# Performance work log

Hardware: AMD Instinct MI355X
Metric: run time of the kernel (lower is better)

## Reference

```python
import jax, jax.numpy as jnp
import numpy as np

V0 = 32000  # medicine vocab; SOS = V0, END = V0 + 1
E = 1024    # emb_dim


def setup_inputs() -> dict:
    key = jax.random.key(0)
    ks = jax.random.split(key, 12)
    s = 0.02
    return {
        "input_diagnosis": jax.random.randint(ks[0], (128,), 0, 35501),
        "input_procedure": jax.random.randint(ks[1], (64,), 0, 35501),
        "input_medicine": jax.random.randint(ks[2], (128,), 0, 35501),
        "dec_tokens": jax.random.randint(ks[3], (64,), 0, V0),
        "enc_emb": jax.random.normal(ks[4], (35501, E), jnp.float32) * s,
        "dec_emb": jax.random.normal(ks[5], (V0 + 2, E), jnp.float32) * s,
        "attn_w": jax.random.normal(ks[6], (1, 2 * E), jnp.float32) * s,
        "attn_b": jnp.zeros((1,), jnp.float32),
        "gru_w_ih": jax.random.normal(ks[7], (3 * E, 2 * E), jnp.float32) * s,
        "gru_w_hh": jax.random.normal(ks[8], (3 * E, E), jnp.float32) * s,
        "gru_b_ih": jnp.zeros((3 * E,), jnp.float32),
        "gru_b_hh": jnp.zeros((3 * E,), jnp.float32),
        "out_w": jax.random.normal(ks[9], (V0 + 2, E), jnp.float32) * s,
        "out_b": jnp.zeros((V0 + 2,), jnp.float32),
    }


def reference(input_diagnosis, input_procedure, input_medicine, dec_tokens,
              enc_emb, dec_emb, attn_w, attn_b,
              gru_w_ih, gru_w_hh, gru_b_ih, gru_b_hh, out_w, out_b):
    # Context: concat of the three code-set embeddings -> [L, E]
    ctx = jnp.concatenate([enc_emb[input_diagnosis],
                           enc_emb[input_procedure],
                           enc_emb[input_medicine]], axis=0)
    # Teacher-forced decoder token sequence: [SOS] + targets -> [T]
    tokens = jnp.concatenate([jnp.array([V0], dec_tokens.dtype), dec_tokens])
    dec_x = dec_emb[tokens]  # [T, E]
    h0 = dec_x[0]            # hidden init = SOS embedding (hidden_state None branch)
    # Additive attention Linear(2E,1): split weight into hidden part / context part
    w_h = attn_w[0, :E]
    w_e = attn_w[0, E:]
    ctx_score = ctx @ w_e + attn_b[0]  # [L], precomputed once

    def step(h, x):
        scores = ctx_score + jnp.dot(h, w_h)          # [L]
        a = jax.nn.softmax(scores)
        c = a @ ctx                                    # [E] weighted context
        u = jnp.concatenate([c, x])                    # [2E] GRU input
        gi = gru_w_ih @ u + gru_b_ih
        gh = gru_w_hh @ h + gru_b_hh
        ir, iz, in_ = jnp.split(gi, 3)
        hr, hz, hn = jnp.split(gh, 3)
        r = jax.nn.sigmoid(ir + hr)
        z = jax.nn.sigmoid(iz + hz)
        n = jnp.tanh(in_ + r * hn)
        h_new = (1.0 - z) * n + z * h                  # PyTorch GRU cell
        logits = out_w @ jax.nn.relu(h_new) + out_b    # [V0+2]
        return h_new, logits

    _, logits = jax.lax.scan(step, h0, dec_x)          # [T, V0+2]
    return logits
```

## Files before the change

### kernel.cpp

```cpp
#include <hip/hip_runtime.h>
#include <hip/hip_cooperative_groups.h>

typedef unsigned long long u64;
#define V0TOK 32000
#define EDIM  1024

__device__ __forceinline__ float dot4(float4 a, float4 b) {
    return fmaf(a.x, b.x, fmaf(a.y, b.y, fmaf(a.z, b.z, a.w * b.w)));
}

__global__ __launch_bounds__(512, 1) void k_rnn(
    const int* __restrict__ diag, const int* __restrict__ proc,
    const int* __restrict__ med,  const int* __restrict__ dtok,
    const float* __restrict__ enc, const float* __restrict__ dec,
    const float* __restrict__ attw,
    const float* __restrict__ wih, const float* __restrict__ whh,
    const float* __restrict__ bih, const float* __restrict__ bhh,
    float* __restrict__ ctx_ws, float* __restrict__ c_ws,
    u64* __restrict__ hbuf, float* __restrict__ hrelu)
{
    const int b = blockIdx.x, tid = threadIdx.x;
    const int w = tid >> 6, l = tid & 63;

    __shared__ float Wx[24 * 1024];
    __shared__ float sm[320];
    __shared__ float red1[8], red2[8];
    __shared__ float hlds[1024];

    if (b < 4)
        __hip_atomic_store(&hbuf[b * 512 + tid], 0ull,
                           __ATOMIC_RELAXED, __HIP_MEMORY_SCOPE_AGENT);
    if (b < 40) {
        int i = 8*b + w;
        int ridx = (i < 128) ? diag[i] : (i < 192 ? proc[i-128] : med[i-192]);
        const float4* row = (const float4*)(enc + (size_t)ridx * EDIM);
        const float4* we  = (const float4*)(attw + EDIM);
        float p = 0.f;
        #pragma unroll
        for (int m = 0; m < 4; m++) p += dot4(row[l + 64*m], we[l + 64*m]);
        #pragma unroll
        for (int off = 32; off; off >>= 1) p += __shfl_xor(p, off);
        if (l == 0) ctx_ws[i] = p;
    }
    __threadfence();
    cooperative_groups::this_grid().sync();
    __threadfence();

    {
        float s1 = (tid < 320) ? ctx_ws[tid] : -1e30f;
        float mx = s1;
        #pragma unroll
        for (int off = 32; off; off >>= 1) mx = fmaxf(mx, __shfl_xor(mx, off));
        if (l == 0) red1[w] = mx;
        __syncthreads();
        mx = red1[0];
        #pragma unroll
        for (int k = 1; k < 8; k++) mx = fmaxf(mx, red1[k]);
        float e1 = (tid < 320) ? expf(s1 - mx) : 0.f;
        float ss = e1;
        #pragma unroll
        for (int off = 32; off; off >>= 1) ss += __shfl_xor(ss, off);
        if (l == 0) red2[w] = ss;
        __syncthreads();
        float tot = red2[0];
        #pragma unroll
        for (int k = 1; k < 8; k++) tot += red2[k];
        if (tid < 320) sm[tid] = e1 / tot;
        __syncthreads();

        int e = 8*b + w;
        float p = 0.f;
        for (int i = l; i < 320; i += 64) {
            int ridx = (i < 128) ? diag[i] : (i < 192 ? proc[i-128] : med[i-192]);
            p += sm[i] * enc[(size_t)ridx * EDIM + e];
        }
        #pragma unroll
        for (int off = 32; off; off >>= 1) p += __shfl_xor(p, off);
        if (l == 0) c_ws[e] = p;
    }
    __threadfence();
    cooperative_groups::this_grid().sync();
    __threadfence();

    const int jr = 8*b + w, jz = 1024 + jr, jn = 2048 + jr;

    {
        const float4* s_r = (const float4*)(wih + (size_t)jr * 2048 + 1024);
        const float4* s_z = (const float4*)(wih + (size_t)jz * 2048 + 1024);
        const float4* s_n = (const float4*)(wih + (size_t)jn * 2048 + 1024);
        float4* d_r = (float4*)(Wx + (0*8 + w) * 1024);
        float4* d_z = (float4*)(Wx + (1*8 + w) * 1024);
        float4* d_n = (float4*)(Wx + (2*8 + w) * 1024);
        #pragma unroll
        for (int m = 0; m < 4; m++) {
            d_r[l + 64*m] = s_r[l + 64*m];
            d_z[l + 64*m] = s_z[l + 64*m];
            d_n[l + 64*m] = s_n[l + 64*m];
        }
    }

    float4 whr[4], whz[4], whn[4];
    {
        const float4* qr = (const float4*)(whh + (size_t)jr * 1024);
        const float4* qz = (const float4*)(whh + (size_t)jz * 1024);
        const float4* qn = (const float4*)(whh + (size_t)jn * 1024);
        #pragma unroll
        for (int m = 0; m < 4; m++) { whr[m] = qr[l + 64*m]; whz[m] = qz[l + 64*m]; whn[m] = qn[l + 64*m]; }
    }

    float4 c4[4], h4[4];
    {
        const float4* cp = (const float4*)c_ws;
        const float4* hp = (const float4*)(dec + (size_t)V0TOK * EDIM);
        #pragma unroll
        for (int m = 0; m < 4; m++) { c4[m] = cp[l + 64*m]; h4[m] = hp[l + 64*m]; }
    }
    const float b_r  = bih[jr] + bhh[jr];
    const float b_z  = bih[jz] + bhh[jz];
    const float b_ni = bih[jn];
    const float b_nh = bhh[jn];

    float gic_r = 0.f, gic_z = 0.f, gic_n = 0.f;
    {
        const float4* pr = (const float4*)(wih + (size_t)jr * 2048);
        const float4* pz = (const float4*)(wih + (size_t)jz * 2048);
        const float4* pn = (const float4*)(wih + (size_t)jn * 2048);
        #pragma unroll
        for (int m = 0; m < 4; m++) {
            gic_r += dot4(pr[l + 64*m], c4[m]);
            gic_z += dot4(pz[l + 64*m], c4[m]);
            gic_n += dot4(pn[l + 64*m], c4[m]);
        }
    }

    __syncthreads();

    const float4* WxR = (const float4*)(Wx + (0*8 + w) * 1024);
    const float4* WxZ = (const float4*)(Wx + (1*8 + w) * 1024);
    const float4* WxN = (const float4*)(Wx + (2*8 + w) * 1024);

    int tokreg = dtok[l];

    float gxr = gic_r, gxz = gic_z, gxn = gic_n;
    #pragma unroll
    for (int m = 0; m < 4; m++) {
        gxr += dot4(WxR[l + 64*m], h4[m]);
        gxz += dot4(WxZ[l + 64*m], h4[m]);
        gxn += dot4(WxN[l + 64*m], h4[m]);
    }
    float4 xv[4];
    {
        int tok1 = __shfl(tokreg, 0);
        const float4* xp = (const float4*)(dec + (size_t)tok1 * EDIM);
        #pragma unroll
        for (int m = 0; m < 4; m++) xv[m] = xp[l + 64*m];
    }

    const int jmi = jr >> 8, jli = (jr >> 2) & 63, jci = jr & 3;

    for (int t = 0; t < 65; t++) {
        float hr = 0.f, hz = 0.f, hn_ = 0.f;
        #pragma unroll
        for (int m = 0; m < 4; m++) {
            hr  += dot4(whr[m], h4[m]);
            hz  += dot4(whz[m], h4[m]);
            hn_ += dot4(whn[m], h4[m]);
        }
        float sr = gxr + hr, sz = gxz + hz, sni = gxn, snh = hn_;
        #pragma unroll
        for (int off = 32; off; off >>= 1) {
            sr  += __shfl_xor(sr, off);  sz  += __shfl_xor(sz, off);
            sni += __shfl_xor(sni, off); snh += __shfl_xor(snh, off);
        }
        float rg = 1.f / (1.f + expf(-(sr + b_r)));
        float zg = 1.f / (1.f + expf(-(sz + b_z)));
        float ng = tanhf(sni + b_ni + rg * (snh + b_nh));

        float4 hs = (jmi == 0) ? h4[0] : (jmi == 1) ? h4[1] : (jmi == 2) ? h4[2] : h4[3];
        float hv0 = (jci == 0) ? hs.x : (jci == 1) ? hs.y : (jci == 2) ? hs.z : hs.w;
        float hv = __shfl(hv0, jli);
        float hnew = (1.f - zg) * ng + zg * hv;

        if (t < 64) {
            const int par = (t + 1) & 1;
            const unsigned tag = (unsigned)(t + 1);
            if (l == 0) {
                hrelu[t * 1024 + jr] = fmaxf(hnew, 0.f);
                u64 pk = ((u64)tag << 32) | (u64)__float_as_uint(hnew);
                __hip_atomic_store(&hbuf[par * 1024 + jr], pk,
                                   __ATOMIC_RELAXED, __HIP_MEMORY_SCOPE_AGENT);
            }

            gxr = gic_r; gxz = gic_z; gxn = gic_n;
            #pragma unroll
            for (int m = 0; m < 4; m++) {
                gxr += dot4(WxR[l + 64*m], xv[m]);
                gxz += dot4(WxZ[l + 64*m], xv[m]);
                gxn += dot4(WxN[l + 64*m], xv[m]);
            }
            if (t < 63) {
                int tok = __shfl(tokreg, t + 1);
                const float4* xp = (const float4*)(dec + (size_t)tok * EDIM);
                #pragma unroll
                for (int m = 0; m < 4; m++) xv[m] = xp[l + 64*m];
            }

            {
                u64* hb = hbuf + par * 1024;
                u64 va, vb2;
                while (1) {
                    va  = __hip_atomic_load(&hb[2*tid],     __ATOMIC_RELAXED, __HIP_MEMORY_SCOPE_AGENT);
                    vb2 = __hip_atomic_load(&hb[2*tid + 1], __ATOMIC_RELAXED, __HIP_MEMORY_SCOPE_AGENT);
                    if (((unsigned)(va >> 32) == tag) & ((unsigned)(vb2 >> 32) == tag)) break;
                }
                hlds[2*tid]     = __uint_as_float((unsigned)va);
                hlds[2*tid + 1] = __uint_as_float((unsigned)vb2);
            }
            __syncthreads();
            #pragma unroll
            for (int m = 0; m < 4; m++) h4[m] = ((const float4*)hlds)[l + 64*m];
            __syncthreads();
        } else {
            if (l == 0) hrelu[64 * 1024 + jr] = fmaxf(hnew, 0.f);
        }
    }
}

__global__ __launch_bounds__(256, 4) void k_logits(
    const float* __restrict__ wo, const float* __restrict__ bo,
    const float* __restrict__ hrelu, float* __restrict__ out)
{
    __shared__ float Hs[65 * 68];
    const int tid = threadIdx.x, q = tid & 15, vl = tid >> 4;
    const int v0 = blockIdx.x * 16;
    const int v  = v0 + vl;
    const int vc = (v < 32002) ? v : 32001;
    const float* wrow = wo + (size_t)vc * 1024;

    float acc[65];
    #pragma unroll
    for (int t = 0; t < 65; t++) acc[t] = 0.f;

    float4 st0, st1, st2, st3, st4;
    #define ISSUE(kc_) do {                                                   \
        int base = (kc_) * 64;                                                \
        { int idx = tid;       st0 = *(const float4*)(hrelu + (idx>>4)*1024 + base + 4*(idx&15)); } \
        { int idx = tid + 256; st1 = *(const float4*)(hrelu + (idx>>4)*1024 + base + 4*(idx&15)); } \
        { int idx = tid + 512; st2 = *(const float4*)(hrelu + (idx>>4)*1024 + base + 4*(idx&15)); } \
        { int idx = tid + 768; st3 = *(const float4*)(hrelu + (idx>>4)*1024 + base + 4*(idx&15)); } \
        if (tid < 16) st4 = *(const float4*)(hrelu + 64*1024 + base + 4*tid); \
    } while (0)
    #define WRITE() do {                                                      \
        { int idx = tid;       *(float4*)(Hs + (idx>>4)*68 + 4*(idx&15)) = st0; } \
        { int idx = tid + 256; *(float4*)(Hs + (idx>>4)*68 + 4*(idx&15)) = st1; } \
        { int idx = tid + 512; *(float4*)(Hs + (idx>>4)*68 + 4*(idx&15)) = st2; } \
        { int idx = tid + 768; *(float4*)(Hs + (idx>>4)*68 + 4*(idx&15)) = st3; } \
        if (tid < 16) *(float4*)(Hs + 64*68 + 4*tid) = st4;                   \
    } while (0)

    ISSUE(0);
    float4 wv = *(const float4*)(wrow + 4*q);

    for (int kc = 0; kc < 16; kc++) {
        WRITE();
        __syncthreads();
        float4 wnext;
        if (kc < 15) {
            ISSUE(kc + 1);
            wnext = *(const float4*)(wrow + (kc + 1) * 64 + 4*q);
        }
        const float* hp = Hs + 4*q;
        #pragma unroll
        for (int t = 0; t < 65; t++) {
            float4 h4 = *(const float4*)(hp + t * 68);
            acc[t] = fmaf(wv.x, h4.x, acc[t]);
            acc[t] = fmaf(wv.y, h4.y, acc[t]);
            acc[t] = fmaf(wv.z, h4.z, acc[t]);
            acc[t] = fmaf(wv.w, h4.w, acc[t]);
        }
        wv = wnext;
        __syncthreads();
    }

    float* Os = Hs;
    #pragma unroll
    for (int t = 0; t < 65; t++) {
        float s_ = acc[t];
        s_ += __shfl_xor(s_, 1);
        s_ += __shfl_xor(s_, 2);
        s_ += __shfl_xor(s_, 4);
        s_ += __shfl_xor(s_, 8);
        if (q == 0) Os[t * 17 + vl] = s_;
    }
    __syncthreads();
    for (int idx = tid; idx < 65 * 16; idx += 256) {
        int t = idx >> 4, c = idx & 15;
        int vv = v0 + c;
        if (vv < 32002) out[(size_t)t * 32002 + vv] = Os[t * 17 + c] + bo[vv];
    }
}

extern "C" void kernel_launch(void* const* d_in, const int* in_sizes, int n_in,
                              void* d_out, int out_size, void* d_ws, size_t ws_size,
                              hipStream_t stream) {
    const int*   diag = (const int*)d_in[0];
    const int*   proc = (const int*)d_in[1];
    const int*   med  = (const int*)d_in[2];
    const int*   dtok = (const int*)d_in[3];
    const float* enc  = (const float*)d_in[4];
    const float* dec  = (const float*)d_in[5];
    const float* attw = (const float*)d_in[6];
    const float* wih  = (const float*)d_in[8];
    const float* whh  = (const float*)d_in[9];
    const float* bih  = (const float*)d_in[10];
    const float* bhh  = (const float*)d_in[11];
    const float* wo   = (const float*)d_in[12];
    const float* bo   = (const float*)d_in[13];
    float* out = (float*)d_out;

    float* ctx_ws = (float*)d_ws;
    float* c_ws   = (float*)((char*)d_ws + 2048);
    u64*   hbuf   = (u64*)  ((char*)d_ws + 16384);
    float* hrelu  = (float*)((char*)d_ws + 32768);

    void* args[] = { (void*)&diag, (void*)&proc, (void*)&med, (void*)&dtok,
                     (void*)&enc, (void*)&dec, (void*)&attw,
                     (void*)&wih, (void*)&whh, (void*)&bih, (void*)&bhh,
                     (void*)&ctx_ws, (void*)&c_ws, (void*)&hbuf, (void*)&hrelu };
    hipLaunchCooperativeKernel((void*)k_rnn, dim3(128), dim3(512), args, 0, stream);

    k_logits<<<dim3(2001), dim3(256), 0, stream>>>(wo, bo, hrelu, out);
}
```

Before: 461.5 us.

## Relay hidden state via per-XCC staging buffer and retile logits kernel

Blocks read the XCC ID from a hardware register. The first eight blocks poll the global hidden-state buffer and copy it into a staging buffer owned by their XCC, while the other blocks spin on that XCC-local copy, with a bounded-iteration fallback to the global buffer. The goal is to cut cross-die coherent polling traffic in the recurrent step and to drop one barrier per step. Separately, the logits kernel gives each thread 4 vocab rows by about 17 timesteps instead of 1 row by 65, which reuses each hidden load across rows and lowers register pressure. The relay depends on the eight lead blocks landing on distinct XCCs and uses plain volatile loads, so correctness and coherence rest on the hardware placement and the fallback path.

Result: slower. 1.106 ms (+139.7%).

```diff
diff --git a/kernel.cpp b/kernel.cpp
--- a/kernel.cpp
+++ b/kernel.cpp
@@ -17,10 +17,17 @@
     const float* __restrict__ wih, const float* __restrict__ whh,
     const float* __restrict__ bih, const float* __restrict__ bhh,
     float* __restrict__ ctx_ws, float* __restrict__ c_ws,
-    u64* __restrict__ hbuf, float* __restrict__ hrelu)
+    u64* __restrict__ hbuf, float* __restrict__ hrelu,
+    u64* __restrict__ stg)
 {
     const int b = blockIdx.x, tid = threadIdx.x;
     const int w = tid >> 6, l = tid & 63;
+
+    unsigned xcc;
+    asm("s_getreg_b32 %0, hwreg(HW_REG_XCC_ID)" : "=s"(xcc));
+    xcc &= 7;
+    u64* stg_x = stg + (size_t)xcc * 2048;
+    const bool lead = (b < 8);
 
     __shared__ float Wx[24 * 1024];
     __shared__ float sm[320];
@@ -30,6 +37,8 @@
     if (b < 4)
         __hip_atomic_store(&hbuf[b * 512 + tid], 0ull,
                            __ATOMIC_RELAXED, __HIP_MEMORY_SCOPE_AGENT);
+    #pragma unroll
+    for (int m = 0; m < 4; m++) stg_x[tid + 512 * m] = 0ull;
     if (b < 40) {
         int i = 8*b + w;
         int ridx = (i < 128) ? diag[i] : (i < 192 ? proc[i-128] : med[i-192]);
@@ -157,6 +166,8 @@
     }
 
     const int jmi = jr >> 8, jli = (jr >> 2) & 63, jci = jr & 3;
+
+    bool fb = false;
 
     for (int t = 0; t < 65; t++) {
         float hr = 0.f, hz = 0.f, hn_ = 0.f;
@@ -205,21 +216,44 @@
                 for (int m = 0; m < 4; m++) xv[m] = xp[l + 64*m];
             }
 
-            {
+            u64 va, vb2;
+            if (lead) {
                 u64* hb = hbuf + par * 1024;
-                u64 va, vb2;
                 while (1) {
                     va  = __hip_atomic_load(&hb[2*tid],     __ATOMIC_RELAXED, __HIP_MEMORY_SCOPE_AGENT);
                     vb2 = __hip_atomic_load(&hb[2*tid + 1], __ATOMIC_RELAXED, __HIP_MEMORY_SCOPE_AGENT);
                     if (((unsigned)(va >> 32) == tag) & ((unsigned)(vb2 >> 32) == tag)) break;
                 }
-                hlds[2*tid]     = __uint_as_float((unsigned)va);
-                hlds[2*tid + 1] = __uint_as_float((unsigned)vb2);
-            }
+                u64* sp = stg_x + (size_t)par * 1024;
+                sp[2*tid]     = va;
+                sp[2*tid + 1] = vb2;
+                __syncthreads();
+            } else {
+                bool got = false;
+                if (!fb) {
+                    volatile const u64* sp = stg_x + (size_t)par * 1024;
+                    for (int it = 0; it < 8192; ++it) {
+                        va  = sp[2*tid];
+                        vb2 = sp[2*tid + 1];
+                        if (((unsigned)(va >> 32) == tag) & ((unsigned)(vb2 >> 32) == tag)) { got = true; break; }
+                    }
+                }
+                int allgot = __syncthreads_and(got ? 1 : 0);
+                if (!allgot) {
+                    fb = true;
+                    u64* hb = hbuf + par * 1024;
+                    while (1) {
+                        va  = __hip_atomic_load(&hb[2*tid],     __ATOMIC_RELAXED, __HIP_MEMORY_SCOPE_AGENT);
+                        vb2 = __hip_atomic_load(&hb[2*tid + 1], __ATOMIC_RELAXED, __HIP_MEMORY_SCOPE_AGENT);
+                        if (((unsigned)(va >> 32) == tag) & ((unsigned)(vb2 >> 32) == tag)) break;
+                    }
+                }
+            }
+            hlds[2*tid]     = __uint_as_float((unsigned)va);
+            hlds[2*tid + 1] = __uint_as_float((unsigned)vb2);
             __syncthreads();
             #pragma unroll
             for (int m = 0; m < 4; m++) h4[m] = ((const float4*)hlds)[l + 64*m];
-            __syncthreads();
         } else {
             if (l == 0) hrelu[64 * 1024 + jr] = fmaxf(hnew, 0.f);
         }
@@ -231,15 +265,23 @@
     const float* __restrict__ hrelu, float* __restrict__ out)
 {
     __shared__ float Hs[65 * 68];
-    const int tid = threadIdx.x, q = tid & 15, vl = tid >> 4;
+    const int tid = threadIdx.x;
+    const int q = tid & 15, vl = (tid >> 4) & 3, s = tid >> 6;
     const int v0 = blockIdx.x * 16;
-    const int v  = v0 + vl;
-    const int vc = (v < 32002) ? v : 32001;
-    const float* wrow = wo + (size_t)vc * 1024;
-
-    float acc[65];
-    #pragma unroll
-    for (int t = 0; t < 65; t++) acc[t] = 0.f;
+    const int T0 = (s == 0) ? 0 : (1 + 16 * s);
+
+    const float* wrow[4];
+    #pragma unroll
+    for (int r = 0; r < 4; r++) {
+        int v = v0 + vl + 4*r;
+        wrow[r] = wo + (size_t)((v < 32002) ? v : 32001) * 1024;
+    }
+
+    float acc[4][17];
+    #pragma unroll
+    for (int r = 0; r < 4; r++)
+        #pragma unroll
+        for (int ti = 0; ti < 17; ti++) acc[r][ti] = 0.f;
 
     float4 st0, st1, st2, st3, st4;
     #define ISSUE(kc_) do {                                                   \
@@ -259,38 +301,47 @@
     } while (0)
 
     ISSUE(0);
-    float4 wv = *(const float4*)(wrow + 4*q);
 
     for (int kc = 0; kc < 16; kc++) {
         WRITE();
         __syncthreads();
-        float4 wnext;
-        if (kc < 15) {
-            ISSUE(kc + 1);
-            wnext = *(const float4*)(wrow + (kc + 1) * 64 + 4*q);
-        }
+        if (kc < 15) ISSUE(kc + 1);
+
+        float4 wv[4];
+        #pragma unroll
+        for (int r = 0; r < 4; r++) wv[r] = *(const float4*)(wrow[r] + kc * 64 + 4*q);
+
         const float* hp = Hs + 4*q;
         #pragma unroll
-        for (int t = 0; t < 65; t++) {
-            float4 h4 = *(const float4*)(hp + t * 68);
-            acc[t] = fmaf(wv.x, h4.x, acc[t]);
-            acc[t] = fmaf(wv.y, h4.y, acc[t]);
-            acc[t] = fmaf(wv.z, h4.z, acc[t]);
-            acc[t] = fmaf(wv.w, h4.w, acc[t]);
-        }
-        wv = wnext;
+        for (int ti = 0; ti < 17; ti++) {
+            if ((ti < 16) | (s == 0)) {
+                float4 h4 = *(const float4*)(hp + (T0 + ti) * 68);
+                #pragma unroll
+                for (int r = 0; r < 4; r++) {
+                    acc[r][ti] = fmaf(wv[r].x, h4.x, acc[r][ti]);
+                    acc[r][ti] = fmaf(wv[r].y, h4.y, acc[r][ti]);
+                    acc[r][ti] = fmaf(wv[r].z, h4.z, acc[r][ti]);
+                    acc[r][ti] = fmaf(wv[r].w, h4.w, acc[r][ti]);
+                }
+            }
+        }
         __syncthreads();
     }
 
     float* Os = Hs;
     #pragma unroll
-    for (int t = 0; t < 65; t++) {
-        float s_ = acc[t];
-        s_ += __shfl_xor(s_, 1);
-        s_ += __shfl_xor(s_, 2);
-        s_ += __shfl_xor(s_, 4);
-        s_ += __shfl_xor(s_, 8);
-        if (q == 0) Os[t * 17 + vl] = s_;
+    for (int ti = 0; ti < 17; ti++) {
+        if ((ti < 16) | (s == 0)) {
+            #pragma unroll
+            for (int r = 0; r < 4; r++) {
+                float s_ = acc[r][ti];
+                s_ += __shfl_xor(s_, 1);
+                s_ += __shfl_xor(s_, 2);
+                s_ += __shfl_xor(s_, 4);
+                s_ += __shfl_xor(s_, 8);
+                if (q == 0) Os[(T0 + ti) * 17 + vl + 4*r] = s_;
+            }
+        }
     }
     __syncthreads();
     for (int idx = tid; idx < 65 * 16; idx += 256) {
@@ -322,11 +373,13 @@
     float* c_ws   = (float*)((char*)d_ws + 2048);
     u64*   hbuf   = (u64*)  ((char*)d_ws + 16384);
     float* hrelu  = (float*)((char*)d_ws + 32768);
+    u64*   stg    = (u64*)  ((char*)d_ws + 299008);
 
     void* args[] = { (void*)&diag, (void*)&proc, (void*)&med, (void*)&dtok,
                      (void*)&enc, (void*)&dec, (void*)&attw,
                      (void*)&wih, (void*)&whh, (void*)&bih, (void*)&bhh,
-                     (void*)&ctx_ws, (void*)&c_ws, (void*)&hbuf, (void*)&hrelu };
+                     (void*)&ctx_ws, (void*)&c_ws, (void*)&hbuf, (void*)&hrelu,
+                     (void*)&stg };
     hipLaunchCooperativeKernel((void*)k_rnn, dim3(128), dim3(512), args, 0, stream);
 
     k_logits<<<dim3(2001), dim3(256), 0, stream>>>(wo, bo, hrelu, out);
```
